# Kernel optimization log

Measured on AMD Instinct MI355X. Metric: run time of the kernel, lower is better.

The kernel has to match this reference:

```python
import jax, jax.numpy as jnp
import numpy as np

B, S, D, H = 4, 2048, 1024, 16
HD = D // H

def setup_inputs() -> dict:
    key = jax.random.key(0)
    ks = jax.random.split(key, 12)
    std = 1.0 / np.sqrt(D)
    inp = {
        'query': jax.random.normal(ks[0], (B, S, D), jnp.float32),
        'key':   jax.random.normal(ks[1], (B, S, D), jnp.float32),
        'value': jax.random.normal(ks[2], (B, S, D), jnp.float32),
        'mask':  jnp.tril(jnp.ones((S, S), jnp.int32))[None, None, :, :],  # [1,1,S,S] causal
        'Wq': jax.random.uniform(ks[3], (D, D), jnp.float32, -std, std),
        'bq': jax.random.uniform(ks[4], (D,), jnp.float32, -std, std),
        'Wk': jax.random.uniform(ks[5], (D, D), jnp.float32, -std, std),
        'bk': jax.random.uniform(ks[6], (D,), jnp.float32, -std, std),
        'Wv': jax.random.uniform(ks[7], (D, D), jnp.float32, -std, std),
        'bv': jax.random.uniform(ks[8], (D,), jnp.float32, -std, std),
        'Wo': jax.random.uniform(ks[9], (D, D), jnp.float32, -std, std),
        'bo': jax.random.uniform(ks[10], (D,), jnp.float32, -std, std),
    }
    return inp

def _split_heads(x, W, b):
    # torch Linear: x @ W.T + b ; then [B,S,H,HD] -> [B,H,S,HD]
    y = jnp.einsum('bsd,ed->bse', x, W) + b
    return y.reshape(x.shape[0], -1, H, HD).transpose(0, 2, 1, 3)

def reference(query, key, value, mask, Wq, bq, Wk, bk, Wv, bv, Wo, bo):
    q = _split_heads(query, Wq, bq)   # [B,H,S,HD]
    k = _split_heads(key,   Wk, bk)
    v = _split_heads(value, Wv, bv)
    logits = jnp.einsum('bhqd,bhkd->bhqk', q, k) / np.sqrt(HD)  # [B,H,S,S]
    logits = jnp.where(mask == 0, jnp.float32(-1e9), logits)
    attn = jax.nn.softmax(logits, axis=-1)
    out = jnp.einsum('bhqk,bhkd->bhqd', attn, v)               # [B,H,S,HD]
    out = out.transpose(0, 2, 1, 3).reshape(query.shape[0], -1, D)
    return jnp.einsum('bsd,ed->bse', out, Wo) + bo
```

## Files before the change

kernel.cpp:

```cpp
#include <hip/hip_runtime.h>
#include <hip/hip_bf16.h>


#define SLEN 2048
#define DMOD 1024

typedef __attribute__((ext_vector_type(8))) short s16x8;
typedef __attribute__((ext_vector_type(4))) float f32x4;

__device__ __forceinline__ unsigned short f2bf(float f) {
    union { __hip_bfloat16 h; unsigned short u; } cv;
    cv.h = __float2bfloat16(f);
    return cv.u;
}
__device__ __forceinline__ unsigned cvtpk(float a, float b) {
    unsigned r;
    asm("v_cvt_pk_bf16_f32 %0, %1, %2" : "=v"(r) : "v"(a), "v"(b));
    return r;
}

__device__ __forceinline__ void gload_lds16(const void* g, void* l) {
    __builtin_amdgcn_global_load_lds(
        (const __attribute__((address_space(1))) void*)g,
        (__attribute__((address_space(3))) void*)l, 16, 0, 0);
}

__global__ __launch_bounds__(256) void convert_bf16(
    const float* __restrict__ q, const float* __restrict__ k,
    const float* __restrict__ v, const float* __restrict__ wq,
    const float* __restrict__ wk, const float* __restrict__ wv,
    const float* __restrict__ wo, unsigned short* __restrict__ ws)
{
    const int bid = blockIdx.x, tid = threadIdx.x;
    const float* src;
    unsigned short* dst;
    size_t off;
    if (bid < 3072) {
        const int t = bid >> 10;
        src = (t == 0) ? q : (t == 1) ? k : v;
        dst = ws + (size_t)t * 8388608;
        off = (size_t)(bid & 1023) * 8192;
    } else {
        const int w = (bid - 3072) >> 7;
        src = (w == 0) ? wq : (w == 1) ? wk : (w == 2) ? wv : wo;
        dst = ws + 25165824 + (size_t)w * 1048576;
        off = (size_t)((bid - 3072) & 127) * 8192;
    }
#pragma unroll
    for (int i = 0; i < 8; ++i) {
        const size_t e = off + (size_t)(i * 256 + tid) * 4;
        float4 x = *reinterpret_cast<const float4*>(&src[e]);
        uint2 u;
        u.x = cvtpk(x.x, x.y);
        u.y = cvtpk(x.z, x.w);
        *reinterpret_cast<uint2*>(&dst[e]) = u;
    }
}

template<int MODE>
__global__ __launch_bounds__(256) void gemm_bf16(
    const unsigned short* __restrict__ A, const unsigned short* __restrict__ W,
    const float* __restrict__ bias, void* __restrict__ outp)
{
    __shared__ unsigned short Asm[2][8192];
    __shared__ unsigned short Bsm[2][8192];

    const int tid  = threadIdx.x;
    const int lane = tid & 63, wid = tid >> 6;
    const int l15 = lane & 15, lhi = lane >> 4;

    const int flat = blockIdx.x;
    const int logical = (flat & 7) * 64 + (flat >> 3);
    const int m0 = (logical >> 3) * 128, n0 = (logical & 7) * 128;

    const int wr = wid >> 1, wc = wid & 1;
    const int srow = lane >> 3;
    const int sgr  = (lane & 7) ^ srow;

    int aoff[2][4], boff[2][4];
#pragma unroll
    for (int kk = 0; kk < 2; ++kk)
#pragma unroll
        for (int i = 0; i < 4; ++i) {
            const int s = ((4 * kk + lhi) ^ (l15 & 7)) * 16;
            aoff[kk][i] = (wr * 64 + i * 16 + l15) * 128 + s;
            boff[kk][i] = (wc * 64 + i * 16 + l15) * 128 + s;
        }

    const unsigned short* apt = A + (size_t)(m0 + wid * 8 + srow) * 1024 + sgr * 8;
    const unsigned short* bpt = W + (size_t)(n0 + wid * 8 + srow) * 1024 + sgr * 8;

    f32x4 acc[4][4];
#pragma unroll
    for (int i = 0; i < 4; ++i)
#pragma unroll
        for (int j = 0; j < 4; ++j) acc[i][j] = (f32x4)0.f;

    auto stage = [&](int bsel) {
        char* ad = (char*)Asm + bsel * 16384 + wid * 1024;
        char* bd = (char*)Bsm + bsel * 16384 + wid * 1024;
#pragma unroll
        for (int i = 0; i < 4; ++i) {
            gload_lds16(apt + i * 32768, ad + i * 4096);
            gload_lds16(bpt + i * 32768, bd + i * 4096);
        }
        apt += 64; bpt += 64;
    };

    stage(0);
    __syncthreads();
    int cur = 0;
#pragma unroll 1
    for (int kt = 0; kt < 16; ++kt) {
        if (kt < 15) stage(cur ^ 1);
        const char* AB = (const char*)Asm + cur * 16384;
        const char* BB = (const char*)Bsm + cur * 16384;
#pragma unroll
        for (int kk = 0; kk < 2; ++kk) {
            s16x8 af[4], bfv[4];
#pragma unroll
            for (int i = 0; i < 4; ++i) af[i]  = *reinterpret_cast<const s16x8*>(AB + aoff[kk][i]);
#pragma unroll
            for (int j = 0; j < 4; ++j) bfv[j] = *reinterpret_cast<const s16x8*>(BB + boff[kk][j]);
#pragma unroll
            for (int i = 0; i < 4; ++i)
#pragma unroll
                for (int j = 0; j < 4; ++j)
                    acc[i][j] = __builtin_amdgcn_mfma_f32_16x16x32_bf16(af[i], bfv[j], acc[i][j], 0, 0, 0);
        }
        __syncthreads();
        cur ^= 1;
    }

#pragma unroll
    for (int j = 0; j < 4; ++j) {
        const int col = n0 + wc * 64 + j * 16 + l15;
        const float bv = bias[col];
#pragma unroll
        for (int i = 0; i < 4; ++i) {
#pragma unroll
            for (int r = 0; r < 4; ++r) {
                const int row = m0 + wr * 64 + i * 16 + lhi * 4 + r;
                const float val = acc[i][j][r] + bv;
                if constexpr (MODE == 2) {
                    ((float*)outp)[(size_t)row * 1024 + col] = val;
                } else if constexpr (MODE == 0) {
                    ((unsigned short*)outp)[(size_t)((row >> 11) * 16 + (col >> 6)) * 131072
                                            + (size_t)(row & 2047) * 64 + (col & 63)] = f2bf(val);
                } else {
                    ((unsigned short*)outp)[(size_t)((row >> 11) * 16 + (col >> 6)) * 131072
                                            + (size_t)(col & 63) * 2048 + (row & 2047)] = f2bf(val);
                }
            }
        }
    }
}

#define EXPC 0.18033688011112043f

__global__ __launch_bounds__(256, 4) void attn_kernel(
    const unsigned short* __restrict__ Q,
    const unsigned short* __restrict__ Kc,
    const unsigned short* __restrict__ Vt,
    unsigned short* __restrict__ Ao)
{
    __shared__ unsigned short Kbuf[2][4096];
    __shared__ unsigned short Vbuf[2][4096];
    __shared__ unsigned short Psm[4][1024];

    const int tid = threadIdx.x, lane = tid & 63, wid = tid >> 6;
    const int l15 = lane & 15, lhi = lane >> 4;
    const int sK = l15 & 7;
    const int sub = lane >> 3, c8s = lane & 7;
    const int thr = wid * 16 + l15;

    int ko[8], pr[2], pw[4];
#pragma unroll
    for (int kk = 0; kk < 2; ++kk) {
        pr[kk] = (l15 * 8 + ((4 * kk + lhi) ^ sK)) * 16;
#pragma unroll
        for (int nb = 0; nb < 4; ++nb)
            ko[kk * 4 + nb] = ((nb * 16 + l15) * 8 + ((4 * kk + lhi) ^ sK)) * 16;
    }
#pragma unroll
    for (int nb = 0; nb < 4; ++nb)
        pw[nb] = (l15 * 16 + ((nb * 4 + lhi) ^ (2 * sK))) * 8;

    const int flat = blockIdx.x;
    const int logical = (flat & 7) * 128 + (flat >> 3);
    const int bx = logical & 15, bh = logical >> 4;

    const size_t base = (size_t)bh * SLEN * 64;
    const unsigned short* Qb = Q + base;
    const unsigned short* Kb = Kc + base;
    const unsigned short* Vb = Vt + base;
    const int b = bh >> 4, h = bh & 15;
    const int scol = (c8s ^ sub) * 8;

    const f32x4 fzero = (f32x4)0.f;
    const s16x8 onesb = (s16x8)(short)0x3F80;

#pragma unroll 1
    for (int seg = 0; seg < 2; ++seg) {
        const int qt = seg ? (31 - bx) : bx;
        const int q0 = qt * 64;

        s16x8 aq[2];
#pragma unroll
        for (int kk = 0; kk < 2; ++kk)
            aq[kk] = *reinterpret_cast<const s16x8*>(
                &Qb[(size_t)(q0 + wid * 16 + l15) * 64 + kk * 32 + 8 * lhi]);

        f32x4 o_acc[4];
#pragma unroll
        for (int nb = 0; nb < 4; ++nb) o_acc[nb] = (f32x4)0.f;
        f32x4 l_acc = (f32x4)0.f;

        const unsigned short* kpt = Kb + (16 * wid + sub) * 64 + scol;
        const unsigned short* vpt = Vb + (size_t)(16 * wid + sub) * SLEN + scol;

        auto stage = [&](int bsel) {
            char* kd = (char*)Kbuf + bsel * 8192 + wid * 2048;
            char* vd = (char*)Vbuf + bsel * 8192 + wid * 2048;
            gload_lds16(kpt,         kd);
            gload_lds16(kpt + 512,   kd + 1024);
            gload_lds16(vpt,         vd);
            gload_lds16(vpt + 16384, vd + 1024);
            kpt += 4096; vpt += 64;
        };

        auto tile = [&](int cbo, bool domask) {
            const char* KB = (const char*)Kbuf + cbo;
            const char* VB = (const char*)Vbuf + cbo;
            char* PW = (char*)Psm + wid * 2048;

            f32x4 sc2[4];
            __builtin_amdgcn_s_setprio(1);
#pragma unroll
            for (int kk = 0; kk < 2; ++kk) {
                s16x8 ak[4];
#pragma unroll
                for (int nb = 0; nb < 4; ++nb)
                    ak[nb] = *reinterpret_cast<const s16x8*>(KB + ko[kk * 4 + nb]);
#pragma unroll
                for (int nb = 0; nb < 4; ++nb)
                    sc2[nb] = __builtin_amdgcn_mfma_f32_16x16x32_bf16(
                        ak[nb], aq[kk], kk == 0 ? fzero : sc2[nb], 0, 0, 0);
            }
            __builtin_amdgcn_s_setprio(0);

            if (domask) {
#pragma unroll
                for (int nb = 0; nb < 4; ++nb)
#pragma unroll
                    for (int r = 0; r < 4; ++r)
                        if (nb * 16 + lhi * 4 + r > thr) sc2[nb][r] = -3e30f;
            }

#pragma unroll
            for (int nb = 0; nb < 4; ++nb) {
                float p0 = exp2f(sc2[nb][0] * EXPC);
                float p1 = exp2f(sc2[nb][1] * EXPC);
                float p2 = exp2f(sc2[nb][2] * EXPC);
                float p3 = exp2f(sc2[nb][3] * EXPC);
                uint2 u;
                u.x = cvtpk(p0, p1);
                u.y = cvtpk(p2, p3);
                *reinterpret_cast<uint2*>(PW + pw[nb]) = u;
            }

            __builtin_amdgcn_s_setprio(1);
#pragma unroll
            for (int kk = 0; kk < 2; ++kk) {
                s16x8 pa = *reinterpret_cast<const s16x8*>(PW + pr[kk]);
                s16x8 bvv[4];
#pragma unroll
                for (int nb = 0; nb < 4; ++nb)
                    bvv[nb] = *reinterpret_cast<const s16x8*>(VB + ko[kk * 4 + nb]);
#pragma unroll
                for (int nb = 0; nb < 4; ++nb)
                    o_acc[nb] = __builtin_amdgcn_mfma_f32_16x16x32_bf16(pa, bvv[nb], o_acc[nb], 0, 0, 0);
                l_acc = __builtin_amdgcn_mfma_f32_16x16x32_bf16(pa, onesb, l_acc, 0, 0, 0);
            }
            __builtin_amdgcn_s_setprio(0);
        };

        stage(0);
        __syncthreads();
        int cur = 0;

#pragma unroll 1
        for (int t = 0; t < qt; ++t) {
            stage(cur ^ 1);
            tile(cur * 8192, false);
            __syncthreads();
            cur ^= 1;
        }
        tile(cur * 8192, true);

        float linv[4];
#pragma unroll
        for (int r = 0; r < 4; ++r) linv[r] = 1.0f / l_acc[r];
#pragma unroll
        for (int nb = 0; nb < 4; ++nb)
#pragma unroll
            for (int r = 0; r < 4; ++r) {
                const int s = q0 + wid * 16 + lhi * 4 + r;
                Ao[((size_t)b * SLEN + s) * DMOD + h * 64 + nb * 16 + l15] =
                    f2bf(o_acc[nb][r] * linv[r]);
            }
        __syncthreads();
    }
}

extern "C" void kernel_launch(void* const* d_in, const int* in_sizes, int n_in,
                              void* d_out, int out_size, void* d_ws, size_t ws_size,
                              hipStream_t stream) {
    const float* q  = (const float*)d_in[0];
    const float* k  = (const float*)d_in[1];
    const float* v  = (const float*)d_in[2];
    const float* Wq = (const float*)d_in[4];
    const float* bq = (const float*)d_in[5];
    const float* Wk = (const float*)d_in[6];
    const float* bk = (const float*)d_in[7];
    const float* Wv = (const float*)d_in[8];
    const float* bv = (const float*)d_in[9];
    const float* Wo = (const float*)d_in[10];
    const float* bo = (const float*)d_in[11];

    unsigned short* wsp = (unsigned short*)d_ws;
    unsigned short* qc  = wsp;
    unsigned short* kc  = wsp + 8388608;
    unsigned short* vc  = wsp + 16777216;
    unsigned short* wqc = wsp + 25165824;
    unsigned short* wkc = wsp + 26214400;
    unsigned short* wvc = wsp + 27262976;
    unsigned short* woc = wsp + 28311552;
    unsigned short* qb  = wsp + 29360128;
    unsigned short* kb  = wsp + 37748736;
    unsigned short* vtb = wsp + 46137344;
    unsigned short* ao  = qc;

    dim3 gb(256);
    convert_bf16<<<dim3(3584), gb, 0, stream>>>(q, k, v, Wq, Wk, Wv, Wo, wsp);
    gemm_bf16<0><<<dim3(512), gb, 0, stream>>>(qc, wqc, bq, qb);
    gemm_bf16<0><<<dim3(512), gb, 0, stream>>>(kc, wkc, bk, kb);
    gemm_bf16<1><<<dim3(512), gb, 0, stream>>>(vc, wvc, bv, vtb);
    attn_kernel<<<dim3(1024), gb, 0, stream>>>(qb, kb, vtb, ao);
    gemm_bf16<2><<<dim3(512), gb, 0, stream>>>(ao, woc, bo, (float*)d_out);
}
```

Measured before the change: 182.0 us.

## Share K/V tile loads between paired low and high query tiles

```diff
diff --git a/kernel.cpp b/kernel.cpp
--- a/kernel.cpp
+++ b/kernel.cpp
@@ -189,6 +189,8 @@
     const int flat = blockIdx.x;
     const int logical = (flat & 7) * 128 + (flat >> 3);
     const int bx = logical & 15, bh = logical >> 4;
+    const int qtL = bx, qtH = 31 - bx;
+    const int q0L = qtL * 64, q0H = qtH * 64;
 
     const size_t base = (size_t)bh * SLEN * 64;
     const unsigned short* Qb = Q + base;
@@ -200,117 +202,117 @@
     const f32x4 fzero = (f32x4)0.f;
     const s16x8 onesb = (s16x8)(short)0x3F80;
 
+    s16x8 aqL[2], aqH[2];
+#pragma unroll
+    for (int kk = 0; kk < 2; ++kk) {
+        aqL[kk] = *reinterpret_cast<const s16x8*>(
+            &Qb[(size_t)(q0L + wid * 16 + l15) * 64 + kk * 32 + 8 * lhi]);
+        aqH[kk] = *reinterpret_cast<const s16x8*>(
+            &Qb[(size_t)(q0H + wid * 16 + l15) * 64 + kk * 32 + 8 * lhi]);
+    }
+
+    f32x4 oL[4], oH[4];
+#pragma unroll
+    for (int nb = 0; nb < 4; ++nb) { oL[nb] = (f32x4)0.f; oH[nb] = (f32x4)0.f; }
+    f32x4 lL = (f32x4)0.f, lH = (f32x4)0.f;
+
+    const unsigned short* kpt = Kb + (16 * wid + sub) * 64 + scol;
+    const unsigned short* vpt = Vb + (size_t)(16 * wid + sub) * SLEN + scol;
+
+    auto stage = [&](int bsel) {
+        char* kd = (char*)Kbuf + bsel * 8192 + wid * 2048;
+        char* vd = (char*)Vbuf + bsel * 8192 + wid * 2048;
+        gload_lds16(kpt,         kd);
+        gload_lds16(kpt + 512,   kd + 1024);
+        gload_lds16(vpt,         vd);
+        gload_lds16(vpt + 16384, vd + 1024);
+        kpt += 4096; vpt += 64;
+    };
+
+    auto tile = [&](s16x8 (&aq)[2], f32x4 (&o_acc)[4], f32x4& l_acc,
+                    bool domask, const char* KB, const char* VB) {
+        char* PW = (char*)Psm + wid * 2048;
+
+        f32x4 sc2[4];
+        __builtin_amdgcn_s_setprio(1);
+#pragma unroll
+        for (int kk = 0; kk < 2; ++kk) {
+            s16x8 ak[4];
+#pragma unroll
+            for (int nb = 0; nb < 4; ++nb)
+                ak[nb] = *reinterpret_cast<const s16x8*>(KB + ko[kk * 4 + nb]);
+#pragma unroll
+            for (int nb = 0; nb < 4; ++nb)
+                sc2[nb] = __builtin_amdgcn_mfma_f32_16x16x32_bf16(
+                    ak[nb], aq[kk], kk == 0 ? fzero : sc2[nb], 0, 0, 0);
+        }
+        __builtin_amdgcn_s_setprio(0);
+
+        if (domask) {
+#pragma unroll
+            for (int nb = 0; nb < 4; ++nb)
+#pragma unroll
+                for (int r = 0; r < 4; ++r)
+                    if (nb * 16 + lhi * 4 + r > thr) sc2[nb][r] = -3e30f;
+        }
+
+#pragma unroll
+        for (int nb = 0; nb < 4; ++nb) {
+            float p0 = exp2f(sc2[nb][0] * EXPC);
+            float p1 = exp2f(sc2[nb][1] * EXPC);
+            float p2 = exp2f(sc2[nb][2] * EXPC);
+            float p3 = exp2f(sc2[nb][3] * EXPC);
+            uint2 u;
+            u.x = cvtpk(p0, p1);
+            u.y = cvtpk(p2, p3);
+            *reinterpret_cast<uint2*>(PW + pw[nb]) = u;
+        }
+
+        __builtin_amdgcn_s_setprio(1);
+#pragma unroll
+        for (int kk = 0; kk < 2; ++kk) {
+            s16x8 pa = *reinterpret_cast<const s16x8*>(PW + pr[kk]);
+            s16x8 bvv[4];
+#pragma unroll
+            for (int nb = 0; nb < 4; ++nb)
+                bvv[nb] = *reinterpret_cast<const s16x8*>(VB + ko[kk * 4 + nb]);
+#pragma unroll
+            for (int nb = 0; nb < 4; ++nb)
+                o_acc[nb] = __builtin_amdgcn_mfma_f32_16x16x32_bf16(pa, bvv[nb], o_acc[nb], 0, 0, 0);
+            l_acc = __builtin_amdgcn_mfma_f32_16x16x32_bf16(pa, onesb, l_acc, 0, 0, 0);
+        }
+        __builtin_amdgcn_s_setprio(0);
+    };
+
+    stage(0);
+    __syncthreads();
+    int cur = 0;
+    const int nt = qtH + 1;
+
 #pragma unroll 1
-    for (int seg = 0; seg < 2; ++seg) {
-        const int qt = seg ? (31 - bx) : bx;
-        const int q0 = qt * 64;
-
-        s16x8 aq[2];
-#pragma unroll
-        for (int kk = 0; kk < 2; ++kk)
-            aq[kk] = *reinterpret_cast<const s16x8*>(
-                &Qb[(size_t)(q0 + wid * 16 + l15) * 64 + kk * 32 + 8 * lhi]);
-
-        f32x4 o_acc[4];
-#pragma unroll
-        for (int nb = 0; nb < 4; ++nb) o_acc[nb] = (f32x4)0.f;
-        f32x4 l_acc = (f32x4)0.f;
-
-        const unsigned short* kpt = Kb + (16 * wid + sub) * 64 + scol;
-        const unsigned short* vpt = Vb + (size_t)(16 * wid + sub) * SLEN + scol;
-
-        auto stage = [&](int bsel) {
-            char* kd = (char*)Kbuf + bsel * 8192 + wid * 2048;
-            char* vd = (char*)Vbuf + bsel * 8192 + wid * 2048;
-            gload_lds16(kpt,         kd);
-            gload_lds16(kpt + 512,   kd + 1024);
-            gload_lds16(vpt,         vd);
-            gload_lds16(vpt + 16384, vd + 1024);
-            kpt += 4096; vpt += 64;
-        };
-
-        auto tile = [&](int cbo, bool domask) {
-            const char* KB = (const char*)Kbuf + cbo;
-            const char* VB = (const char*)Vbuf + cbo;
-            char* PW = (char*)Psm + wid * 2048;
-
-            f32x4 sc2[4];
-            __builtin_amdgcn_s_setprio(1);
-#pragma unroll
-            for (int kk = 0; kk < 2; ++kk) {
-                s16x8 ak[4];
-#pragma unroll
-                for (int nb = 0; nb < 4; ++nb)
-                    ak[nb] = *reinterpret_cast<const s16x8*>(KB + ko[kk * 4 + nb]);
-#pragma unroll
-                for (int nb = 0; nb < 4; ++nb)
-                    sc2[nb] = __builtin_amdgcn_mfma_f32_16x16x32_bf16(
-                        ak[nb], aq[kk], kk == 0 ? fzero : sc2[nb], 0, 0, 0);
-            }
-            __builtin_amdgcn_s_setprio(0);
-
-            if (domask) {
-#pragma unroll
-                for (int nb = 0; nb < 4; ++nb)
-#pragma unroll
-                    for (int r = 0; r < 4; ++r)
-                        if (nb * 16 + lhi * 4 + r > thr) sc2[nb][r] = -3e30f;
-            }
-
-#pragma unroll
-            for (int nb = 0; nb < 4; ++nb) {
-                float p0 = exp2f(sc2[nb][0] * EXPC);
-                float p1 = exp2f(sc2[nb][1] * EXPC);
-                float p2 = exp2f(sc2[nb][2] * EXPC);
-                float p3 = exp2f(sc2[nb][3] * EXPC);
-                uint2 u;
-                u.x = cvtpk(p0, p1);
-                u.y = cvtpk(p2, p3);
-                *reinterpret_cast<uint2*>(PW + pw[nb]) = u;
-            }
-
-            __builtin_amdgcn_s_setprio(1);
-#pragma unroll
-            for (int kk = 0; kk < 2; ++kk) {
-                s16x8 pa = *reinterpret_cast<const s16x8*>(PW + pr[kk]);
-                s16x8 bvv[4];
-#pragma unroll
-                for (int nb = 0; nb < 4; ++nb)
-                    bvv[nb] = *reinterpret_cast<const s16x8*>(VB + ko[kk * 4 + nb]);
-#pragma unroll
-                for (int nb = 0; nb < 4; ++nb)
-                    o_acc[nb] = __builtin_amdgcn_mfma_f32_16x16x32_bf16(pa, bvv[nb], o_acc[nb], 0, 0, 0);
-                l_acc = __builtin_amdgcn_mfma_f32_16x16x32_bf16(pa, onesb, l_acc, 0, 0, 0);
-            }
-            __builtin_amdgcn_s_setprio(0);
-        };
-
-        stage(0);
+    for (int t = 0; t < nt; ++t) {
+        if (t + 1 < nt) stage(cur ^ 1);
+        const char* KB = (const char*)Kbuf + cur * 8192;
+        const char* VB = (const char*)Vbuf + cur * 8192;
+        if (t <= qtL) tile(aqL, oL, lL, t == qtL, KB, VB);
+        tile(aqH, oH, lH, t == qtH, KB, VB);
         __syncthreads();
-        int cur = 0;
-
-#pragma unroll 1
-        for (int t = 0; t < qt; ++t) {
-            stage(cur ^ 1);
-            tile(cur * 8192, false);
-            __syncthreads();
-            cur ^= 1;
-        }
-        tile(cur * 8192, true);
-
-        float linv[4];
-#pragma unroll
-        for (int r = 0; r < 4; ++r) linv[r] = 1.0f / l_acc[r];
-#pragma unroll
-        for (int nb = 0; nb < 4; ++nb)
-#pragma unroll
-            for (int r = 0; r < 4; ++r) {
-                const int s = q0 + wid * 16 + lhi * 4 + r;
-                Ao[((size_t)b * SLEN + s) * DMOD + h * 64 + nb * 16 + l15] =
-                    f2bf(o_acc[nb][r] * linv[r]);
-            }
-        __syncthreads();
-    }
+        cur ^= 1;
+    }
+
+    float liL[4], liH[4];
+#pragma unroll
+    for (int r = 0; r < 4; ++r) { liL[r] = 1.0f / lL[r]; liH[r] = 1.0f / lH[r]; }
+#pragma unroll
+    for (int nb = 0; nb < 4; ++nb)
+#pragma unroll
+        for (int r = 0; r < 4; ++r) {
+            const int sL = q0L + wid * 16 + lhi * 4 + r;
+            const int sH = q0H + wid * 16 + lhi * 4 + r;
+            const size_t cix = h * 64 + nb * 16 + l15;
+            Ao[((size_t)b * SLEN + sL) * DMOD + cix] = f2bf(oL[nb][r] * liL[r]);
+            Ao[((size_t)b * SLEN + sH) * DMOD + cix] = f2bf(oH[nb][r] * liH[r]);
+        }
 }
 
 extern "C" void kernel_launch(void* const* d_in, const int* in_sizes, int n_in,
```

After: 182.0 us. About the same (-0.0%).
